# Performance work log

Measured on AMD Instinct MI355X. Metric: run time of the kernel, lower is better.

## Reference

```python
import jax, jax.numpy as jnp
import numpy as np

B, T, D, H = 8, 1024, 1024, 16
NEG = -1e9  # stands in for -inf in the causal mask (matches float('-inf') semantics under softmax)


def setup_inputs() -> dict:
    key = jax.random.key(0)
    ks = jax.random.split(key, 8)
    s = 0.02
    x = jax.random.normal(ks[0], (B, T, D), dtype=jnp.float32)
    # additive causal mask like whisper: zeros on/below diagonal, -inf above
    mask = jnp.triu(jnp.full((T, T), NEG, dtype=jnp.float32), k=1)
    Wq = jax.random.normal(ks[1], (D, D), dtype=jnp.float32) * s
    bq = jax.random.normal(ks[2], (D,), dtype=jnp.float32) * s
    Wk = jax.random.normal(ks[3], (D, D), dtype=jnp.float32) * s
    Wv = jax.random.normal(ks[4], (D, D), dtype=jnp.float32) * s
    bv = jax.random.normal(ks[5], (D,), dtype=jnp.float32) * s
    Wo = jax.random.normal(ks[6], (D, D), dtype=jnp.float32) * s
    bo = jax.random.normal(ks[7], (D,), dtype=jnp.float32) * s
    return {"x": x, "mask": mask, "Wq": Wq, "bq": bq, "Wk": Wk, "Wv": Wv, "bv": bv, "Wo": Wo, "bo": bo}


def reference(x, mask, Wq, bq, Wk, Wv, bv, Wo, bo):
    n_batch, n_ctx, n_state = x.shape
    head_dim = n_state // H
    scale = head_dim ** (-0.25)

    q = x @ Wq.T + bq            # [B,T,D]
    k = x @ Wk.T                 # key Linear has no bias
    v = x @ Wv.T + bv

    # [B,T,D] -> [B,H,T,hd]
    q = q.reshape(n_batch, n_ctx, H, head_dim).transpose(0, 2, 1, 3) * scale
    kt = k.reshape(n_batch, n_ctx, H, head_dim).transpose(0, 2, 3, 1) * scale  # [B,H,hd,T]
    v = v.reshape(n_batch, n_ctx, H, head_dim).transpose(0, 2, 1, 3)

    qk = jnp.einsum('bhqd,bhdk->bhqk', q, kt) + mask[:n_ctx, :n_ctx]
    w = jax.nn.softmax(qk.astype(jnp.float32), axis=-1).astype(q.dtype)
    wv = jnp.einsum('bhqk,bhkd->bhqd', w, v)  # [B,H,T,hd]
    wv = wv.transpose(0, 2, 1, 3).reshape(n_batch, n_ctx, n_state)
    return wv @ Wo.T + bo
```

## Files before the change

### kernel.cpp

```cpp
#include <hip/hip_runtime.h>
#include <stdint.h>

typedef unsigned short u16;
typedef __attribute__((ext_vector_type(8))) short bf16x8;
typedef __attribute__((ext_vector_type(4))) float f32x4;

__device__ __forceinline__ float b2f(u16 u) {
    union { uint32_t i; float f; } c; c.i = ((uint32_t)u) << 16; return c.f;
}
__device__ __forceinline__ u16 f2b(float f) {
    union { float f; uint32_t i; } c; c.f = f;
    uint32_t u = c.i;
    uint32_t r = (u + 0x7fffu + ((u >> 16) & 1u)) >> 16;
    return (u16)r;
}
__device__ __forceinline__ uint32_t fbits(float f) {
    union { float f; uint32_t u; } c; c.f = f; return c.u;
}

__device__ __forceinline__ void gll16(const u16* g, u16* lds_base) {
    __builtin_amdgcn_global_load_lds(
        (const __attribute__((address_space(1))) uint32_t*)g,
        (__attribute__((address_space(3))) uint32_t*)lds_base, 16, 0, 0);
}

#define GK 1024
#define QSCALE 0.18033688011112042f
#define LDPA 72

__global__ __launch_bounds__(256) void conv_all(
    const void* x, const void* wq, const void* bqp, const void* wk,
    const void* wv, const void* bvp, const void* wo, const void* bop,
    u16* xb, u16* wqb, u16* bqb, u16* wkb, u16* wvb, u16* bvb, u16* wob, u16* bob,
    const u16* __restrict__ sniff)
{
    const bool is_f32 = (sniff[1] == 0);
    const int blk = blockIdx.x;
    const void* s; u16* d; int i0, n;
    if (blk < 4096)      { s = x;   d = xb;  i0 = blk;        n = 8388608; }
    else if (blk < 4608) { s = wq;  d = wqb; i0 = blk - 4096; n = 1048576; }
    else if (blk < 5120) { s = wk;  d = wkb; i0 = blk - 4608; n = 1048576; }
    else if (blk < 5632) { s = wv;  d = wvb; i0 = blk - 5120; n = 1048576; }
    else if (blk < 6144) { s = wo;  d = wob; i0 = blk - 5632; n = 1048576; }
    else if (blk == 6144){ s = bqp; d = bqb; i0 = 0;          n = 1024; }
    else if (blk == 6145){ s = bvp; d = bvb; i0 = 0;          n = 1024; }
    else                 { s = bop; d = bob; i0 = 0;          n = 1024; }
    int i = (i0 * 256 + threadIdx.x) * 8;
    if (i >= n) return;
    if (is_f32) {
        const float* sf = (const float*)s;
        float4 lo = *(const float4*)(sf + i);
        float4 hi = *(const float4*)(sf + i + 4);
        u16 o[8];
        o[0]=f2b(lo.x); o[1]=f2b(lo.y); o[2]=f2b(lo.z); o[3]=f2b(lo.w);
        o[4]=f2b(hi.x); o[5]=f2b(hi.y); o[6]=f2b(hi.z); o[7]=f2b(hi.w);
        *(uint4*)(d + i) = *(const uint4*)o;
    } else {
        *(uint4*)(d + i) = *(const uint4*)((const u16*)s + i);
    }
}


#define NGRAN 3072
#define BOFF  8192

__global__ __launch_bounds__(512, 2) void gemm_qkv(
    const u16* __restrict__ xb, const u16* __restrict__ wcomb,
    const u16* __restrict__ bq, const u16* __restrict__ bv,
    u16* __restrict__ qb, u16* __restrict__ kb, u16* __restrict__ vtb)
{
    __shared__ __align__(16) u16 S[2][NGRAN * 8];

    const int flat = blockIdx.x;
    const int swz = (flat & 7) * 96 + (flat >> 3);
    const int mt = swz & 63, nt = swz >> 6;
    const int m0 = mt * 128;
    const int n0full = nt * 256;

    const int t = threadIdx.x;
    const int lane = t & 63, w = t >> 6;
    const int quad = lane >> 4, l15 = lane & 15;
    const int wm = w >> 2, wn = w & 3;

    const int srow = lane >> 3, scol = (lane & 7) * 8;
    const u16* srcp[6];
    int ldso[6];
#pragma unroll
    for (int L = 0; L < 6; L++) {
        const int c = L * 8 + w;
        ldso[L] = c * 512;
        if (c < 16)  srcp[L] = xb    + (size_t)(m0 + c * 8 + srow) * GK + scol;
        else         srcp[L] = wcomb + (size_t)(n0full + (c - 16) * 8 + srow) * GK + scol;
    }

    f32x4 acc[4][4];
#pragma unroll
    for (int i = 0; i < 4; i++)
#pragma unroll
        for (int j = 0; j < 4; j++)
            acc[i][j] = (f32x4){0.f, 0.f, 0.f, 0.f};

#pragma unroll
    for (int L = 0; L < 6; L++) gll16(srcp[L], &S[0][ldso[L]]);
    asm volatile("s_waitcnt vmcnt(0)" ::: "memory");
    __builtin_amdgcn_s_barrier();
    asm volatile("" ::: "memory");

    for (int tt = 0; tt < 16; ++tt) {
        if (tt < 15) {
            const int k0 = (tt + 1) * 64;
            u16* Sn = &S[(tt + 1) & 1][0];
#pragma unroll
            for (int L = 0; L < 6; L++) gll16(srcp[L] + k0, Sn + ldso[L]);
        }
        const u16* Sb = &S[tt & 1][0];
#pragma unroll
        for (int ks = 0; ks < 2; ks++) {
            bf16x8 af[4], bf[4];
#pragma unroll
            for (int mi = 0; mi < 4; mi++)
                af[mi] = *(const bf16x8*)(Sb + (wm * 64 + mi * 16 + l15) * 64 + ks * 32 + quad * 8);
#pragma unroll
            for (int ni = 0; ni < 4; ni++)
                bf[ni] = *(const bf16x8*)(Sb + BOFF + (wn * 64 + ni * 16 + l15) * 64 + ks * 32 + quad * 8);
            __builtin_amdgcn_s_setprio(1);
#pragma unroll
            for (int mi = 0; mi < 4; mi++)
#pragma unroll
                for (int ni = 0; ni < 4; ni++)
                    acc[mi][ni] = __builtin_amdgcn_mfma_f32_16x16x32_bf16(
                        af[mi], bf[ni], acc[mi][ni], 0, 0, 0);
            __builtin_amdgcn_s_setprio(0);
        }
        asm volatile("s_waitcnt vmcnt(0) lgkmcnt(0)" ::: "memory");
        __builtin_amdgcn_s_barrier();
        asm volatile("" ::: "memory");
    }

    const int which = nt >> 2;
    const int nbase = (nt & 3) * 256 + wn * 64;
#pragma unroll
    for (int mi = 0; mi < 4; mi++)
#pragma unroll
        for (int ni = 0; ni < 4; ni++) {
            const int gn = nbase + ni * 16 + l15;
            const int gm = m0 + wm * 64 + mi * 16 + quad * 4;
            if (which == 2) {
                const int b = gm >> 10, ml = gm & 1023;
                const int h = gn >> 6, dw = gn & 63;
                const float bb = b2f(bv[gn]);
                union { u16 h4[4]; uint2 v; } pk;
#pragma unroll
                for (int r = 0; r < 4; r++)
                    pk.h4[r] = f2b(acc[mi][ni][r] + bb);
                *(uint2*)(vtb + (((size_t)(b * 16 + h) * 64 + dw) << 10) + ml) = pk.v;
            } else if (which == 0) {
                const float bb = b2f(bq[gn]);
#pragma unroll
                for (int r = 0; r < 4; r++)
                    qb[(size_t)(gm + r) * 1024 + gn] = f2b((acc[mi][ni][r] + bb) * QSCALE);
            } else {
#pragma unroll
                for (int r = 0; r < 4; r++)
                    kb[(size_t)(gm + r) * 1024 + gn] = f2b(acc[mi][ni][r]);
            }
        }
}

__global__ __launch_bounds__(512, 2) void gemm_out(
    const u16* __restrict__ A, const u16* __restrict__ W,
    const u16* __restrict__ bias, float* __restrict__ C)
{
    __shared__ __align__(16) u16 S[2][NGRAN * 8];

    const int flat = blockIdx.x;
    const int swz = (flat & 7) * 32 + (flat >> 3);
    const int mt = swz & 63, nt = swz >> 6;
    const int m0 = mt * 128;
    const int n0 = nt * 256;

    const int t = threadIdx.x;
    const int lane = t & 63, w = t >> 6;
    const int quad = lane >> 4, l15 = lane & 15;
    const int wm = w >> 2, wn = w & 3;

    const int srow = lane >> 3, scol = (lane & 7) * 8;
    const u16* srcp[6];
    int ldso[6];
#pragma unroll
    for (int L = 0; L < 6; L++) {
        const int c = L * 8 + w;
        ldso[L] = c * 512;
        if (c < 16)  srcp[L] = A + (size_t)(m0 + c * 8 + srow) * GK + scol;
        else         srcp[L] = W + (size_t)(n0 + (c - 16) * 8 + srow) * GK + scol;
    }

    f32x4 acc[4][4];
#pragma unroll
    for (int i = 0; i < 4; i++)
#pragma unroll
        for (int j = 0; j < 4; j++)
            acc[i][j] = (f32x4){0.f, 0.f, 0.f, 0.f};

#pragma unroll
    for (int L = 0; L < 6; L++) gll16(srcp[L], &S[0][ldso[L]]);
    asm volatile("s_waitcnt vmcnt(0)" ::: "memory");
    __builtin_amdgcn_s_barrier();
    asm volatile("" ::: "memory");

    for (int tt = 0; tt < 16; ++tt) {
        if (tt < 15) {
            const int k0 = (tt + 1) * 64;
            u16* Sn = &S[(tt + 1) & 1][0];
#pragma unroll
            for (int L = 0; L < 6; L++) gll16(srcp[L] + k0, Sn + ldso[L]);
        }
        const u16* Sb = &S[tt & 1][0];
#pragma unroll
        for (int ks = 0; ks < 2; ks++) {
            bf16x8 af[4], bf[4];
#pragma unroll
            for (int mi = 0; mi < 4; mi++)
                af[mi] = *(const bf16x8*)(Sb + (wm * 64 + mi * 16 + l15) * 64 + ks * 32 + quad * 8);
#pragma unroll
            for (int ni = 0; ni < 4; ni++)
                bf[ni] = *(const bf16x8*)(Sb + BOFF + (wn * 64 + ni * 16 + l15) * 64 + ks * 32 + quad * 8);
            __builtin_amdgcn_s_setprio(1);
#pragma unroll
            for (int mi = 0; mi < 4; mi++)
#pragma unroll
                for (int ni = 0; ni < 4; ni++)
                    acc[mi][ni] = __builtin_amdgcn_mfma_f32_16x16x32_bf16(
                        af[mi], bf[ni], acc[mi][ni], 0, 0, 0);
            __builtin_amdgcn_s_setprio(0);
        }
        asm volatile("s_waitcnt vmcnt(0) lgkmcnt(0)" ::: "memory");
        __builtin_amdgcn_s_barrier();
        asm volatile("" ::: "memory");
    }

#pragma unroll
    for (int mi = 0; mi < 4; mi++)
#pragma unroll
        for (int ni = 0; ni < 4; ni++) {
            const int gn = n0 + wn * 64 + ni * 16 + l15;
            const int gm = m0 + wm * 64 + mi * 16 + quad * 4;
            const float bb = b2f(bias[gn]);
#pragma unroll
            for (int r = 0; r < 4; r++)
                C[(size_t)(gm + r) * 1024 + gn] = acc[mi][ni][r] + bb;
        }
}

__global__ __launch_bounds__(512, 4) void attn_kernel(
    const u16* q, const u16* kg, const u16* vt, u16* o)
{
    const int qt = (blockIdx.x + 2 * (blockIdx.y >> 6)) & 3;
    const int bh = blockIdx.y;
    const int b = bh >> 4, h = bh & 15;
    const size_t base = (size_t)b * 1024 * 1024 + (size_t)h * 64;
    const size_t vbase = (size_t)bh * 64 * 1024;

    __shared__ __align__(16) u16 Ks[2][64 * LDPA];
    __shared__ __align__(16) u16 Vs[2][64 * LDPA];
    __shared__ __align__(16) u16 U[256 * LDPA];

    const int t = threadIdx.x;
    const int lane = t & 63, w = t >> 6;
    const int quad = lane >> 4, l15 = lane & 15;

#pragma unroll
    for (int i = 0; i < 4; i++) {
        int idx = i * 512 + t;
        int r = idx >> 3, c = idx & 7;
        *(uint4*)(&U[r * LDPA + c * 8]) =
            *(const uint4*)(q + base + (size_t)(qt * 256 + r) * 1024 + c * 8);
    }
    __syncthreads();
    bf16x8 qf[2][2];
#pragma unroll
    for (int qc = 0; qc < 2; qc++)
#pragma unroll
        for (int ks = 0; ks < 2; ks++)
            qf[qc][ks] = *(const bf16x8*)(&U[(w * 32 + qc * 16 + l15) * LDPA + ks * 32 + quad * 8]);
    __syncthreads();
    u16* Pw = &U[(w * 32) * LDPA];

    const int wqmin = qt * 256 + w * 32;
    float l_[2] = {0.f, 0.f};
    f32x4 accO[2][4];
#pragma unroll
    for (int qc = 0; qc < 2; qc++)
#pragma unroll
        for (int f = 0; f < 4; f++) accO[qc][f] = (f32x4){0.f, 0.f, 0.f, 0.f};

    const int jmax = 4 * qt + 3;
    const int sr = t >> 3, sc = (t & 7) * 8;
    uint4 rK = *(const uint4*)(kg + base + (size_t)sr * 1024 + sc);
    uint4 rV = *(const uint4*)(vt + vbase + (size_t)sr * 1024 + sc);

    for (int j = 0; j <= jmax; j++) {
        const int buf = j & 1;
        *(uint4*)(&Ks[buf][sr * LDPA + sc]) = rK;
        *(uint4*)(&Vs[buf][sr * LDPA + sc]) = rV;
        if (j < jmax) {
            rK = *(const uint4*)(kg + base + (size_t)((j + 1) * 64 + sr) * 1024 + sc);
            rV = *(const uint4*)(vt + vbase + (size_t)sr * 1024 + (j + 1) * 64 + sc);
        }
        __syncthreads();

        if (j * 64 > wqmin + 31) continue;

        f32x4 st[2][4];
#pragma unroll
        for (int qc = 0; qc < 2; qc++)
#pragma unroll
            for (int ni = 0; ni < 4; ni++) st[qc][ni] = (f32x4){0.f, 0.f, 0.f, 0.f};
#pragma unroll
        for (int ks = 0; ks < 2; ks++)
#pragma unroll
            for (int ni = 0; ni < 4; ni++) {
                bf16x8 kf = *(const bf16x8*)(&Ks[buf][(ni * 16 + l15) * LDPA + ks * 32 + quad * 8]);
                st[0][ni] = __builtin_amdgcn_mfma_f32_16x16x32_bf16(kf, qf[0][ks], st[0][ni], 0, 0, 0);
                st[1][ni] = __builtin_amdgcn_mfma_f32_16x16x32_bf16(kf, qf[1][ks], st[1][ni], 0, 0, 0);
            }

        const bool diag = (j * 64 + 63 > wqmin);
#pragma unroll
        for (int qc = 0; qc < 2; qc++) {
            const int q_g = wqmin + qc * 16 + l15;
            float ps = 0.f;
#pragma unroll
            for (int ni = 0; ni < 4; ni++) {
                float p[4];
#pragma unroll
                for (int r = 0; r < 4; r++) {
                    float e = __builtin_amdgcn_exp2f(st[qc][ni][r]);
                    if (diag) {
                        int key_g = j * 64 + ni * 16 + quad * 4 + r;
                        e = (key_g > q_g) ? 0.f : e;
                    }
                    p[r] = e;
                    ps += e;
                }
                uint2 pkv;
                pkv.x = __builtin_amdgcn_perm(fbits(p[1]) + 0x8000u, fbits(p[0]) + 0x8000u, 0x07060302u);
                pkv.y = __builtin_amdgcn_perm(fbits(p[3]) + 0x8000u, fbits(p[2]) + 0x8000u, 0x07060302u);
                *(uint2*)(&Pw[(qc * 16 + l15) * LDPA + ni * 16 + quad * 4]) = pkv;
            }
            l_[qc] += ps;
        }

#pragma unroll
        for (int ks = 0; ks < 2; ks++) {
            bf16x8 pf0 = *(const bf16x8*)(&Pw[(l15) * LDPA + ks * 32 + quad * 8]);
            bf16x8 pf1 = *(const bf16x8*)(&Pw[(16 + l15) * LDPA + ks * 32 + quad * 8]);
#pragma unroll
            for (int f = 0; f < 4; f++) {
                bf16x8 vf = *(const bf16x8*)(&Vs[buf][(f * 16 + l15) * LDPA + ks * 32 + quad * 8]);
                accO[0][f] = __builtin_amdgcn_mfma_f32_16x16x32_bf16(vf, pf0, accO[0][f], 0, 0, 0);
                accO[1][f] = __builtin_amdgcn_mfma_f32_16x16x32_bf16(vf, pf1, accO[1][f], 0, 0, 0);
            }
        }
    }

#pragma unroll
    for (int qc = 0; qc < 2; qc++) {
        float l = l_[qc];
        l += __shfl_xor(l, 16, 64);
        l += __shfl_xor(l, 32, 64);
        float inv = 1.0f / l;
        const int q_g = wqmin + qc * 16 + l15;
#pragma unroll
        for (int f = 0; f < 4; f++) {
            union { u16 h4[4]; uint2 v; } pk;
#pragma unroll
            for (int r = 0; r < 4; r++) pk.h4[r] = f2b(accO[qc][f][r] * inv);
            *(uint2*)(o + base + (size_t)q_g * 1024 + f * 16 + quad * 4) = pk.v;
        }
    }
}

extern "C" void kernel_launch(void* const* d_in, const int* in_sizes, int n_in,
                              void* d_out, int out_size, void* d_ws, size_t ws_size,
                              hipStream_t stream) {
    const u16* mask = (const u16*)d_in[1];

    const size_t MT = (size_t)8192 * 1024;
    const size_t WT = (size_t)1024 * 1024;
    u16* ws  = (u16*)d_ws;
    u16* xb  = ws;
    u16* qb  = xb + MT;
    u16* kb  = qb + MT;
    u16* vtb = kb + MT;
    u16* wqb = vtb + MT;
    u16* wkb = wqb + WT;
    u16* wvb = wkb + WT;
    u16* wob = wvb + WT;
    u16* bqb = wob + WT;
    u16* bvb = bqb + 1024;
    u16* bob = bvb + 1024;

    hipLaunchKernelGGL(conv_all, dim3(6147), dim3(256), 0, stream,
                       d_in[0], d_in[2], d_in[3], d_in[4], d_in[5], d_in[6],
                       d_in[7], d_in[8],
                       xb, wqb, bqb, wkb, wvb, bvb, wob, bob, mask);

    hipLaunchKernelGGL(gemm_qkv, dim3(768), dim3(512), 0, stream,
                       xb, wqb, bqb, bvb, qb, kb, vtb);

    hipLaunchKernelGGL(attn_kernel, dim3(4, 128), dim3(512), 0, stream, qb, kb, vtb, qb);

    hipLaunchKernelGGL(gemm_out, dim3(256), dim3(512), 0, stream,
                       qb, wob, bob, (float*)d_out);
}
```

Before: 252.5 us.

## Restructure projection GEMMs into 4-stage K=32 pipeline with swizzled LDS and 256x128 tiles

Both projection GEMMs now use a 256x128 block tile instead of 128x256 and a K step of 32 instead of 64. They keep a four-buffer LDS ring with three stages in flight, using partial vmcnt waits rather than draining every iteration. LDS rows are XOR-swizzled on both the global-to-LDS writes and the fragment reads to cut bank conflicts. The block-to-tile mapping groups M tiles per XCD for L2 reuse. In exchange there are twice as many barriers per K, and the larger LDS footprint (96KB) may limit occupancy.

```diff
diff --git a/kernel.cpp b/kernel.cpp
--- a/kernel.cpp
+++ b/kernel.cpp
@@ -61,37 +61,39 @@
 }
 
 
-#define NGRAN 3072
-#define BOFF  8192
-
 __global__ __launch_bounds__(512, 2) void gemm_qkv(
     const u16* __restrict__ xb, const u16* __restrict__ wcomb,
     const u16* __restrict__ bq, const u16* __restrict__ bv,
     u16* __restrict__ qb, u16* __restrict__ kb, u16* __restrict__ vtb)
 {
-    __shared__ __align__(16) u16 S[2][NGRAN * 8];
+    __shared__ __align__(16) u16 S[4][12288];
 
     const int flat = blockIdx.x;
-    const int swz = (flat & 7) * 96 + (flat >> 3);
-    const int mt = swz & 63, nt = swz >> 6;
-    const int m0 = mt * 128;
-    const int n0full = nt * 256;
+    const int xcd = flat & 7, pos = flat >> 3;
+    const int nt = pos >> 2;
+    const int mt = xcd * 4 + (pos & 3);
+    const int m0 = mt * 256;
+    const int n0 = nt * 128;
 
     const int t = threadIdx.x;
     const int lane = t & 63, w = t >> 6;
     const int quad = lane >> 4, l15 = lane & 15;
-    const int wm = w >> 2, wn = w & 3;
-
-    const int srow = lane >> 3, scol = (lane & 7) * 8;
-    const u16* srcp[6];
-    int ldso[6];
-#pragma unroll
-    for (int L = 0; L < 6; L++) {
-        const int c = L * 8 + w;
-        ldso[L] = c * 512;
-        if (c < 16)  srcp[L] = xb    + (size_t)(m0 + c * 8 + srow) * GK + scol;
-        else         srcp[L] = wcomb + (size_t)(n0full + (c - 16) * 8 + srow) * GK + scol;
-    }
+    const int wm = w >> 1, wn = w & 1;
+
+    const int srow = lane >> 2;
+    const int gs = (lane & 3) ^ ((lane >> 3) & 3);
+    const u16* srcA0 = xb    + (size_t)(m0 + w * 16 + srow) * GK + gs * 8;
+    const u16* srcA1 = xb    + (size_t)(m0 + 128 + w * 16 + srow) * GK + gs * 8;
+    const u16* srcB  = wcomb + (size_t)(n0 + w * 16 + srow) * GK + gs * 8;
+
+    const int sqx = (quad ^ ((l15 >> 1) & 3)) * 8;
+    int aoff[4], boff[4];
+#pragma unroll
+    for (int mi = 0; mi < 4; mi++)
+        aoff[mi] = (wm * 64 + mi * 16 + l15) * 32 + sqx;
+#pragma unroll
+    for (int ni = 0; ni < 4; ni++)
+        boff[ni] = 8192 + (wn * 64 + ni * 16 + l15) * 32 + sqx;
 
     f32x4 acc[4][4];
 #pragma unroll
@@ -100,45 +102,56 @@
         for (int j = 0; j < 4; j++)
             acc[i][j] = (f32x4){0.f, 0.f, 0.f, 0.f};
 
-#pragma unroll
-    for (int L = 0; L < 6; L++) gll16(srcp[L], &S[0][ldso[L]]);
-    asm volatile("s_waitcnt vmcnt(0)" ::: "memory");
-    __builtin_amdgcn_s_barrier();
-    asm volatile("" ::: "memory");
-
-    for (int tt = 0; tt < 16; ++tt) {
-        if (tt < 15) {
-            const int k0 = (tt + 1) * 64;
-            u16* Sn = &S[(tt + 1) & 1][0];
-#pragma unroll
-            for (int L = 0; L < 6; L++) gll16(srcp[L] + k0, Sn + ldso[L]);
-        }
-        const u16* Sb = &S[tt & 1][0];
-#pragma unroll
-        for (int ks = 0; ks < 2; ks++) {
-            bf16x8 af[4], bf[4];
-#pragma unroll
-            for (int mi = 0; mi < 4; mi++)
-                af[mi] = *(const bf16x8*)(Sb + (wm * 64 + mi * 16 + l15) * 64 + ks * 32 + quad * 8);
+    auto STAGE = [&](int h) {
+        u16* Sn = &S[h & 3][0];
+        const int ko = h * 32;
+        gll16(srcA0 + ko, Sn + w * 512);
+        gll16(srcA1 + ko, Sn + (w + 8) * 512);
+        gll16(srcB  + ko, Sn + 8192 + w * 512);
+    };
+    auto KSTEP = [&](int h, bool doStage) {
+        const u16* Sb = &S[h & 3][0];
+        bf16x8 af[4], bf[4];
+#pragma unroll
+        for (int mi = 0; mi < 4; mi++) af[mi] = *(const bf16x8*)(Sb + aoff[mi]);
+#pragma unroll
+        for (int ni = 0; ni < 4; ni++) bf[ni] = *(const bf16x8*)(Sb + boff[ni]);
+        if (doStage) STAGE(h + 3);
+        asm volatile("s_waitcnt lgkmcnt(0)" ::: "memory");
+        __builtin_amdgcn_sched_barrier(0);
+        __builtin_amdgcn_s_setprio(1);
+#pragma unroll
+        for (int mi = 0; mi < 4; mi++)
 #pragma unroll
             for (int ni = 0; ni < 4; ni++)
-                bf[ni] = *(const bf16x8*)(Sb + BOFF + (wn * 64 + ni * 16 + l15) * 64 + ks * 32 + quad * 8);
-            __builtin_amdgcn_s_setprio(1);
-#pragma unroll
-            for (int mi = 0; mi < 4; mi++)
-#pragma unroll
-                for (int ni = 0; ni < 4; ni++)
-                    acc[mi][ni] = __builtin_amdgcn_mfma_f32_16x16x32_bf16(
-                        af[mi], bf[ni], acc[mi][ni], 0, 0, 0);
-            __builtin_amdgcn_s_setprio(0);
-        }
-        asm volatile("s_waitcnt vmcnt(0) lgkmcnt(0)" ::: "memory");
+                acc[mi][ni] = __builtin_amdgcn_mfma_f32_16x16x32_bf16(
+                    af[mi], bf[ni], acc[mi][ni], 0, 0, 0);
+        __builtin_amdgcn_s_setprio(0);
+    };
+
+    STAGE(0); STAGE(1); STAGE(2);
+    asm volatile("s_waitcnt vmcnt(6)" ::: "memory");
+    __builtin_amdgcn_s_barrier();
+    asm volatile("" ::: "memory");
+
+    for (int h = 0; h < 29; ++h) {
+        KSTEP(h, true);
+        asm volatile("s_waitcnt vmcnt(6)" ::: "memory");
         __builtin_amdgcn_s_barrier();
         asm volatile("" ::: "memory");
     }
-
-    const int which = nt >> 2;
-    const int nbase = (nt & 3) * 256 + wn * 64;
+    KSTEP(29, false);
+    asm volatile("s_waitcnt vmcnt(3)" ::: "memory");
+    __builtin_amdgcn_s_barrier();
+    asm volatile("" ::: "memory");
+    KSTEP(30, false);
+    asm volatile("s_waitcnt vmcnt(0)" ::: "memory");
+    __builtin_amdgcn_s_barrier();
+    asm volatile("" ::: "memory");
+    KSTEP(31, false);
+
+    const int which = nt >> 3;
+    const int nbase = (nt & 7) * 128 + wn * 64;
 #pragma unroll
     for (int mi = 0; mi < 4; mi++)
 #pragma unroll
@@ -171,29 +184,34 @@
     const u16* __restrict__ A, const u16* __restrict__ W,
     const u16* __restrict__ bias, float* __restrict__ C)
 {
-    __shared__ __align__(16) u16 S[2][NGRAN * 8];
+    __shared__ __align__(16) u16 S[4][12288];
 
     const int flat = blockIdx.x;
-    const int swz = (flat & 7) * 32 + (flat >> 3);
-    const int mt = swz & 63, nt = swz >> 6;
-    const int m0 = mt * 128;
-    const int n0 = nt * 256;
+    const int xcd = flat & 7, pos = flat >> 3;
+    const int nt = pos >> 2;
+    const int mt = xcd * 4 + (pos & 3);
+    const int m0 = mt * 256;
+    const int n0 = nt * 128;
 
     const int t = threadIdx.x;
     const int lane = t & 63, w = t >> 6;
     const int quad = lane >> 4, l15 = lane & 15;
-    const int wm = w >> 2, wn = w & 3;
-
-    const int srow = lane >> 3, scol = (lane & 7) * 8;
-    const u16* srcp[6];
-    int ldso[6];
-#pragma unroll
-    for (int L = 0; L < 6; L++) {
-        const int c = L * 8 + w;
-        ldso[L] = c * 512;
-        if (c < 16)  srcp[L] = A + (size_t)(m0 + c * 8 + srow) * GK + scol;
-        else         srcp[L] = W + (size_t)(n0 + (c - 16) * 8 + srow) * GK + scol;
-    }
+    const int wm = w >> 1, wn = w & 1;
+
+    const int srow = lane >> 2;
+    const int gs = (lane & 3) ^ ((lane >> 3) & 3);
+    const u16* srcA0 = A + (size_t)(m0 + w * 16 + srow) * GK + gs * 8;
+    const u16* srcA1 = A + (size_t)(m0 + 128 + w * 16 + srow) * GK + gs * 8;
+    const u16* srcB  = W + (size_t)(n0 + w * 16 + srow) * GK + gs * 8;
+
+    const int sqx = (quad ^ ((l15 >> 1) & 3)) * 8;
+    int aoff[4], boff[4];
+#pragma unroll
+    for (int mi = 0; mi < 4; mi++)
+        aoff[mi] = (wm * 64 + mi * 16 + l15) * 32 + sqx;
+#pragma unroll
+    for (int ni = 0; ni < 4; ni++)
+        boff[ni] = 8192 + (wn * 64 + ni * 16 + l15) * 32 + sqx;
 
     f32x4 acc[4][4];
 #pragma unroll
@@ -202,42 +220,53 @@
         for (int j = 0; j < 4; j++)
             acc[i][j] = (f32x4){0.f, 0.f, 0.f, 0.f};
 
-#pragma unroll
-    for (int L = 0; L < 6; L++) gll16(srcp[L], &S[0][ldso[L]]);
-    asm volatile("s_waitcnt vmcnt(0)" ::: "memory");
-    __builtin_amdgcn_s_barrier();
-    asm volatile("" ::: "memory");
-
-    for (int tt = 0; tt < 16; ++tt) {
-        if (tt < 15) {
-            const int k0 = (tt + 1) * 64;
-            u16* Sn = &S[(tt + 1) & 1][0];
-#pragma unroll
-            for (int L = 0; L < 6; L++) gll16(srcp[L] + k0, Sn + ldso[L]);
-        }
-        const u16* Sb = &S[tt & 1][0];
-#pragma unroll
-        for (int ks = 0; ks < 2; ks++) {
-            bf16x8 af[4], bf[4];
-#pragma unroll
-            for (int mi = 0; mi < 4; mi++)
-                af[mi] = *(const bf16x8*)(Sb + (wm * 64 + mi * 16 + l15) * 64 + ks * 32 + quad * 8);
+    auto STAGE = [&](int h) {
+        u16* Sn = &S[h & 3][0];
+        const int ko = h * 32;
+        gll16(srcA0 + ko, Sn + w * 512);
+        gll16(srcA1 + ko, Sn + (w + 8) * 512);
+        gll16(srcB  + ko, Sn + 8192 + w * 512);
+    };
+    auto KSTEP = [&](int h, bool doStage) {
+        const u16* Sb = &S[h & 3][0];
+        bf16x8 af[4], bf[4];
+#pragma unroll
+        for (int mi = 0; mi < 4; mi++) af[mi] = *(const bf16x8*)(Sb + aoff[mi]);
+#pragma unroll
+        for (int ni = 0; ni < 4; ni++) bf[ni] = *(const bf16x8*)(Sb + boff[ni]);
+        if (doStage) STAGE(h + 3);
+        asm volatile("s_waitcnt lgkmcnt(0)" ::: "memory");
+        __builtin_amdgcn_sched_barrier(0);
+        __builtin_amdgcn_s_setprio(1);
+#pragma unroll
+        for (int mi = 0; mi < 4; mi++)
 #pragma unroll
             for (int ni = 0; ni < 4; ni++)
-                bf[ni] = *(const bf16x8*)(Sb + BOFF + (wn * 64 + ni * 16 + l15) * 64 + ks * 32 + quad * 8);
-            __builtin_amdgcn_s_setprio(1);
-#pragma unroll
-            for (int mi = 0; mi < 4; mi++)
-#pragma unroll
-                for (int ni = 0; ni < 4; ni++)
-                    acc[mi][ni] = __builtin_amdgcn_mfma_f32_16x16x32_bf16(
-                        af[mi], bf[ni], acc[mi][ni], 0, 0, 0);
-            __builtin_amdgcn_s_setprio(0);
-        }
-        asm volatile("s_waitcnt vmcnt(0) lgkmcnt(0)" ::: "memory");
+                acc[mi][ni] = __builtin_amdgcn_mfma_f32_16x16x32_bf16(
+                    af[mi], bf[ni], acc[mi][ni], 0, 0, 0);
+        __builtin_amdgcn_s_setprio(0);
+    };
+
+    STAGE(0); STAGE(1); STAGE(2);
+    asm volatile("s_waitcnt vmcnt(6)" ::: "memory");
+    __builtin_amdgcn_s_barrier();
+    asm volatile("" ::: "memory");
+
+    for (int h = 0; h < 29; ++h) {
+        KSTEP(h, true);
+        asm volatile("s_waitcnt vmcnt(6)" ::: "memory");
         __builtin_amdgcn_s_barrier();
         asm volatile("" ::: "memory");
     }
+    KSTEP(29, false);
+    asm volatile("s_waitcnt vmcnt(3)" ::: "memory");
+    __builtin_amdgcn_s_barrier();
+    asm volatile("" ::: "memory");
+    KSTEP(30, false);
+    asm volatile("s_waitcnt vmcnt(0)" ::: "memory");
+    __builtin_amdgcn_s_barrier();
+    asm volatile("" ::: "memory");
+    KSTEP(31, false);
 
 #pragma unroll
     for (int mi = 0; mi < 4; mi++)
```

New measurement: 232.7 us. -7.9%, faster.

## Use 256x256 GEMM tiles with XOR-swizzled LDS and multi-stage prefetch pipeline

Applied to the files above, without the earlier changes.

Both projection GEMMs move from 128x256 to 256x256 output tiles per block, so each wave holds an 8x4 accumulator grid and operand reuse per LDS load goes up. K-slices are staged as 32-wide half-tiles into an 8-slot LDS ring with an XOR chunk swizzle to avoid bank conflicts. Loads are issued several stages ahead with partial vmcnt waits and a barrier per phase, instead of a full drain each iteration. The cost is half as many blocks (384 and 128 on a 256-CU part, which hurts load balance for the output GEMM), 128 KB of LDS per block, and higher register pressure.

```diff
diff --git a/kernel.cpp b/kernel.cpp
--- a/kernel.cpp
+++ b/kernel.cpp
@@ -61,90 +61,121 @@
 }
 
 
-#define NGRAN 3072
-#define BOFF  8192
+#define VM6 asm volatile("s_waitcnt vmcnt(6)" ::: "memory")
+#define VM4 asm volatile("s_waitcnt vmcnt(4)" ::: "memory")
+#define VM0 asm volatile("s_waitcnt vmcnt(0)" ::: "memory")
+#define BARR do { __builtin_amdgcn_s_barrier(); asm volatile("" ::: "memory"); } while(0)
+
+#define PHASE(Q, BUF, DO_STAGE, UU)                                            \
+  {                                                                            \
+    const u16* Sa = &S[(((BUF) << 2) | (((Q) >> 1) << 1))][0];                 \
+    bf16x8 af0 = *(const bf16x8*)(Sa + aoff[((Q)&1)*4 + 0]);                   \
+    bf16x8 af1 = *(const bf16x8*)(Sa + aoff[((Q)&1)*4 + 1]);                   \
+    bf16x8 af2 = *(const bf16x8*)(Sa + aoff[((Q)&1)*4 + 2]);                   \
+    bf16x8 af3 = *(const bf16x8*)(Sa + aoff[((Q)&1)*4 + 3]);                   \
+    if (((Q) & 1) == 0) {                                                      \
+      const u16* Sbp = Sa + 8192;                                              \
+      bfr[0] = *(const bf16x8*)(Sbp + boff[0]);                                \
+      bfr[1] = *(const bf16x8*)(Sbp + boff[1]);                                \
+      bfr[2] = *(const bf16x8*)(Sbp + boff[2]);                                \
+      bfr[3] = *(const bf16x8*)(Sbp + boff[3]);                                \
+    }                                                                          \
+    if (DO_STAGE) STAGE(UU);                                                   \
+    asm volatile("s_waitcnt lgkmcnt(0)" ::: "memory");                         \
+    __builtin_amdgcn_sched_barrier(0);                                         \
+    __builtin_amdgcn_s_setprio(1);                                             \
+    _Pragma("unroll")                                                          \
+    for (int jj = 0; jj < 4; jj++) {                                           \
+      acc[((Q)&1)*4+0][jj] = __builtin_amdgcn_mfma_f32_16x16x32_bf16(af0, bfr[jj], acc[((Q)&1)*4+0][jj], 0,0,0); \
+      acc[((Q)&1)*4+1][jj] = __builtin_amdgcn_mfma_f32_16x16x32_bf16(af1, bfr[jj], acc[((Q)&1)*4+1][jj], 0,0,0); \
+      acc[((Q)&1)*4+2][jj] = __builtin_amdgcn_mfma_f32_16x16x32_bf16(af2, bfr[jj], acc[((Q)&1)*4+2][jj], 0,0,0); \
+      acc[((Q)&1)*4+3][jj] = __builtin_amdgcn_mfma_f32_16x16x32_bf16(af3, bfr[jj], acc[((Q)&1)*4+3][jj], 0,0,0); \
+    }                                                                          \
+    __builtin_amdgcn_s_setprio(0);                                             \
+  }
 
 __global__ __launch_bounds__(512, 2) void gemm_qkv(
     const u16* __restrict__ xb, const u16* __restrict__ wcomb,
     const u16* __restrict__ bq, const u16* __restrict__ bv,
     u16* __restrict__ qb, u16* __restrict__ kb, u16* __restrict__ vtb)
 {
-    __shared__ __align__(16) u16 S[2][NGRAN * 8];
+    __shared__ __align__(16) u16 S[8][8192];
 
     const int flat = blockIdx.x;
-    const int swz = (flat & 7) * 96 + (flat >> 3);
-    const int mt = swz & 63, nt = swz >> 6;
-    const int m0 = mt * 128;
-    const int n0full = nt * 256;
-
-    const int t = threadIdx.x;
-    const int lane = t & 63, w = t >> 6;
+    const int xcd = flat & 7, pos = flat >> 3;
+    const int mt = xcd * 4 + (pos & 3);
+    const int nt = pos >> 2;
+    const int m0 = mt * 256;
+    const int n0 = nt * 256;
+
+    const int tid = threadIdx.x;
+    const int lane = tid & 63, w = tid >> 6;
     const int quad = lane >> 4, l15 = lane & 15;
     const int wm = w >> 2, wn = w & 3;
 
-    const int srow = lane >> 3, scol = (lane & 7) * 8;
-    const u16* srcp[6];
-    int ldso[6];
-#pragma unroll
-    for (int L = 0; L < 6; L++) {
-        const int c = L * 8 + w;
-        ldso[L] = c * 512;
-        if (c < 16)  srcp[L] = xb    + (size_t)(m0 + c * 8 + srow) * GK + scol;
-        else         srcp[L] = wcomb + (size_t)(n0full + (c - 16) * 8 + srow) * GK + scol;
-    }
-
-    f32x4 acc[4][4];
-#pragma unroll
-    for (int i = 0; i < 4; i++)
+    const int srow = tid >> 2;
+    const int chk = (tid & 3) ^ ((tid >> 3) & 3);
+    const u16* pA1 = xb    + (size_t)(m0 + srow) * GK + chk * 8;
+    const u16* pA2 = xb    + (size_t)(m0 + 128 + srow) * GK + chk * 8;
+    const u16* pB1 = wcomb + (size_t)(n0 + srow) * GK + chk * 8;
+    const u16* pB2 = wcomb + (size_t)(n0 + 128 + srow) * GK + chk * 8;
+
+    const int cq = (quad ^ ((l15 >> 1) & 3)) * 8;
+    int aoff[8], boff[4];
+#pragma unroll
+    for (int mf = 0; mf < 8; mf++)
+        aoff[mf] = (wm * 128 + mf * 16 + l15) * 32 + cq;
+#pragma unroll
+    for (int nf = 0; nf < 4; nf++)
+        boff[nf] = (wn * 64 + nf * 16 + l15) * 32 + cq;
+
+    f32x4 acc[8][4];
+#pragma unroll
+    for (int i = 0; i < 8; i++)
 #pragma unroll
         for (int j = 0; j < 4; j++)
             acc[i][j] = (f32x4){0.f, 0.f, 0.f, 0.f};
-
-#pragma unroll
-    for (int L = 0; L < 6; L++) gll16(srcp[L], &S[0][ldso[L]]);
-    asm volatile("s_waitcnt vmcnt(0)" ::: "memory");
-    __builtin_amdgcn_s_barrier();
-    asm volatile("" ::: "memory");
-
-    for (int tt = 0; tt < 16; ++tt) {
-        if (tt < 15) {
-            const int k0 = (tt + 1) * 64;
-            u16* Sn = &S[(tt + 1) & 1][0];
-#pragma unroll
-            for (int L = 0; L < 6; L++) gll16(srcp[L] + k0, Sn + ldso[L]);
-        }
-        const u16* Sb = &S[tt & 1][0];
-#pragma unroll
-        for (int ks = 0; ks < 2; ks++) {
-            bf16x8 af[4], bf[4];
-#pragma unroll
-            for (int mi = 0; mi < 4; mi++)
-                af[mi] = *(const bf16x8*)(Sb + (wm * 64 + mi * 16 + l15) * 64 + ks * 32 + quad * 8);
-#pragma unroll
-            for (int ni = 0; ni < 4; ni++)
-                bf[ni] = *(const bf16x8*)(Sb + BOFF + (wn * 64 + ni * 16 + l15) * 64 + ks * 32 + quad * 8);
-            __builtin_amdgcn_s_setprio(1);
-#pragma unroll
-            for (int mi = 0; mi < 4; mi++)
-#pragma unroll
-                for (int ni = 0; ni < 4; ni++)
-                    acc[mi][ni] = __builtin_amdgcn_mfma_f32_16x16x32_bf16(
-                        af[mi], bf[ni], acc[mi][ni], 0, 0, 0);
-            __builtin_amdgcn_s_setprio(0);
-        }
-        asm volatile("s_waitcnt vmcnt(0) lgkmcnt(0)" ::: "memory");
-        __builtin_amdgcn_s_barrier();
-        asm volatile("" ::: "memory");
-    }
+    bf16x8 bfr[4];
+
+    auto STAGE = [&](int U) {
+        const int tau = U >> 2, ty = U & 3;
+        const int ko = tau * 64 + (ty >> 1) * 32;
+        u16* d = &S[((tau & 1) << 2) | ty][w * 512];
+        const u16* s1 = (ty & 1) ? pB1 : pA1;
+        const u16* s2 = (ty & 1) ? pB2 : pA2;
+        gll16(s1 + ko, d);
+        gll16(s2 + ko, d + 4096);
+    };
+
+    STAGE(0); STAGE(1); STAGE(2); STAGE(3); STAGE(4);
+    VM6; BARR;
+
+#pragma unroll 1
+    for (int it = 0; it < 14; ++it) {
+        const int buf = it & 1;
+        const int U0 = it * 4 + 5;
+        PHASE(0, buf, true, U0);           BARR;
+        PHASE(1, buf, true, U0 + 1);  VM6; BARR;
+        PHASE(2, buf, true, U0 + 2);       BARR;
+        PHASE(3, buf, true, U0 + 3);  VM6; BARR;
+    }
+    PHASE(0, 0, true, 61);       BARR;
+    PHASE(1, 0, true, 62);  VM6; BARR;
+    PHASE(2, 0, true, 63);       BARR;
+    PHASE(3, 0, false, 0);  VM4; BARR;
+    PHASE(0, 1, false, 0);       BARR;
+    PHASE(1, 1, false, 0);  VM0; BARR;
+    PHASE(2, 1, false, 0);       BARR;
+    PHASE(3, 1, false, 0);
 
     const int which = nt >> 2;
     const int nbase = (nt & 3) * 256 + wn * 64;
 #pragma unroll
-    for (int mi = 0; mi < 4; mi++)
+    for (int mi = 0; mi < 8; mi++)
 #pragma unroll
         for (int ni = 0; ni < 4; ni++) {
             const int gn = nbase + ni * 16 + l15;
-            const int gm = m0 + wm * 64 + mi * 16 + quad * 4;
+            const int gm = m0 + wm * 128 + mi * 16 + quad * 4;
             if (which == 2) {
                 const int b = gm >> 10, ml = gm & 1023;
                 const int h = gn >> 6, dw = gn & 63;
@@ -171,80 +202,81 @@
     const u16* __restrict__ A, const u16* __restrict__ W,
     const u16* __restrict__ bias, float* __restrict__ C)
 {
-    __shared__ __align__(16) u16 S[2][NGRAN * 8];
+    __shared__ __align__(16) u16 S[8][8192];
 
     const int flat = blockIdx.x;
-    const int swz = (flat & 7) * 32 + (flat >> 3);
-    const int mt = swz & 63, nt = swz >> 6;
-    const int m0 = mt * 128;
+    const int xcd = flat & 7, pos = flat >> 3;
+    const int mt = xcd * 4 + (pos & 3);
+    const int nt = pos >> 2;
+    const int m0 = mt * 256;
     const int n0 = nt * 256;
 
-    const int t = threadIdx.x;
-    const int lane = t & 63, w = t >> 6;
+    const int tid = threadIdx.x;
+    const int lane = tid & 63, w = tid >> 6;
     const int quad = lane >> 4, l15 = lane & 15;
     const int wm = w >> 2, wn = w & 3;
 
-    const int srow = lane >> 3, scol = (lane & 7) * 8;
-    const u16* srcp[6];
-    int ldso[6];
-#pragma unroll
-    for (int L = 0; L < 6; L++) {
-        const int c = L * 8 + w;
-        ldso[L] = c * 512;
-        if (c < 16)  srcp[L] = A + (size_t)(m0 + c * 8 + srow) * GK + scol;
-        else         srcp[L] = W + (size_t)(n0 + (c - 16) * 8 + srow) * GK + scol;
-    }
-
-    f32x4 acc[4][4];
-#pragma unroll
-    for (int i = 0; i < 4; i++)
+    const int srow = tid >> 2;
+    const int chk = (tid & 3) ^ ((tid >> 3) & 3);
+    const u16* pA1 = A + (size_t)(m0 + srow) * GK + chk * 8;
+    const u16* pA2 = A + (size_t)(m0 + 128 + srow) * GK + chk * 8;
+    const u16* pB1 = W + (size_t)(n0 + srow) * GK + chk * 8;
+    const u16* pB2 = W + (size_t)(n0 + 128 + srow) * GK + chk * 8;
+
+    const int cq = (quad ^ ((l15 >> 1) & 3)) * 8;
+    int aoff[8], boff[4];
+#pragma unroll
+    for (int mf = 0; mf < 8; mf++)
+        aoff[mf] = (wm * 128 + mf * 16 + l15) * 32 + cq;
+#pragma unroll
+    for (int nf = 0; nf < 4; nf++)
+        boff[nf] = (wn * 64 + nf * 16 + l15) * 32 + cq;
+
+    f32x4 acc[8][4];
+#pragma unroll
+    for (int i = 0; i < 8; i++)
 #pragma unroll
         for (int j = 0; j < 4; j++)
             acc[i][j] = (f32x4){0.f, 0.f, 0.f, 0.f};
-
-#pragma unroll
-    for (int L = 0; L < 6; L++) gll16(srcp[L], &S[0][ldso[L]]);
-    asm volatile("s_waitcnt vmcnt(0)" ::: "memory");
-    __builtin_amdgcn_s_barrier();
-    asm volatile("" ::: "memory");
-
-    for (int tt = 0; tt < 16; ++tt) {
-        if (tt < 15) {
-            const int k0 = (tt + 1) * 64;
-            u16* Sn = &S[(tt + 1) & 1][0];
-#pragma unroll
-            for (int L = 0; L < 6; L++) gll16(srcp[L] + k0, Sn + ldso[L]);
-        }
-        const u16* Sb = &S[tt & 1][0];
-#pragma unroll
-        for (int ks = 0; ks < 2; ks++) {
-            bf16x8 af[4], bf[4];
-#pragma unroll
-            for (int mi = 0; mi < 4; mi++)
-                af[mi] = *(const bf16x8*)(Sb + (wm * 64 + mi * 16 + l15) * 64 + ks * 32 + quad * 8);
-#pragma unroll
-            for (int ni = 0; ni < 4; ni++)
-                bf[ni] = *(const bf16x8*)(Sb + BOFF + (wn * 64 + ni * 16 + l15) * 64 + ks * 32 + quad * 8);
-            __builtin_amdgcn_s_setprio(1);
-#pragma unroll
-            for (int mi = 0; mi < 4; mi++)
-#pragma unroll
-                for (int ni = 0; ni < 4; ni++)
-                    acc[mi][ni] = __builtin_amdgcn_mfma_f32_16x16x32_bf16(
-                        af[mi], bf[ni], acc[mi][ni], 0, 0, 0);
-            __builtin_amdgcn_s_setprio(0);
-        }
-        asm volatile("s_waitcnt vmcnt(0) lgkmcnt(0)" ::: "memory");
-        __builtin_amdgcn_s_barrier();
-        asm volatile("" ::: "memory");
-    }
-
-#pragma unroll
-    for (int mi = 0; mi < 4; mi++)
+    bf16x8 bfr[4];
+
+    auto STAGE = [&](int U) {
+        const int tau = U >> 2, ty = U & 3;
+        const int ko = tau * 64 + (ty >> 1) * 32;
+        u16* d = &S[((tau & 1) << 2) | ty][w * 512];
+        const u16* s1 = (ty & 1) ? pB1 : pA1;
+        const u16* s2 = (ty & 1) ? pB2 : pA2;
+        gll16(s1 + ko, d);
+        gll16(s2 + ko, d + 4096);
+    };
+
+    STAGE(0); STAGE(1); STAGE(2); STAGE(3); STAGE(4);
+    VM6; BARR;
+
+#pragma unroll 1
+    for (int it = 0; it < 14; ++it) {
+        const int buf = it & 1;
+        const int U0 = it * 4 + 5;
+        PHASE(0, buf, true, U0);           BARR;
+        PHASE(1, buf, true, U0 + 1);  VM6; BARR;
+        PHASE(2, buf, true, U0 + 2);       BARR;
+        PHASE(3, buf, true, U0 + 3);  VM6; BARR;
+    }
+    PHASE(0, 0, true, 61);       BARR;
+    PHASE(1, 0, true, 62);  VM6; BARR;
+    PHASE(2, 0, true, 63);       BARR;
+    PHASE(3, 0, false, 0);  VM4; BARR;
+    PHASE(0, 1, false, 0);       BARR;
+    PHASE(1, 1, false, 0);  VM0; BARR;
+    PHASE(2, 1, false, 0);       BARR;
+    PHASE(3, 1, false, 0);
+
+#pragma unroll
+    for (int mi = 0; mi < 8; mi++)
 #pragma unroll
         for (int ni = 0; ni < 4; ni++) {
             const int gn = n0 + wn * 64 + ni * 16 + l15;
-            const int gm = m0 + wm * 64 + mi * 16 + quad * 4;
+            const int gm = m0 + wm * 128 + mi * 16 + quad * 4;
             const float bb = b2f(bias[gn]);
 #pragma unroll
             for (int r = 0; r < 4; r++)
@@ -406,11 +438,11 @@
                        d_in[7], d_in[8],
                        xb, wqb, bqb, wkb, wvb, bvb, wob, bob, mask);
 
-    hipLaunchKernelGGL(gemm_qkv, dim3(768), dim3(512), 0, stream,
+    hipLaunchKernelGGL(gemm_qkv, dim3(384), dim3(512), 0, stream,
                        xb, wqb, bqb, bvb, qb, kb, vtb);
 
     hipLaunchKernelGGL(attn_kernel, dim3(4, 128), dim3(512), 0, stream, qb, kb, vtb, qb);
 
-    hipLaunchKernelGGL(gemm_out, dim3(256), dim3(512), 0, stream,
+    hipLaunchKernelGGL(gemm_out, dim3(128), dim3(512), 0, stream,
                        qb, wob, bob, (float*)d_out);
 }
```

New measurement: 244.1 us. 1.03x faster.
